# Kernel optimization log

Measured on AMD Instinct MI355X. Metric: run time of the kernel, lower is better.

The kernel has to match this reference:

```python
import jax, jax.numpy as jnp
import numpy as np

N_NODES = 100000
N_EDGES = 1600000
D_IN = 64
D_OUT = 64


def setup_inputs() -> dict:
    key = jax.random.key(0)
    k1, k2, k3, k4 = jax.random.split(key, 4)
    feat = jax.random.normal(k1, (N_NODES, D_IN), dtype=jnp.float32)
    edge_src = jax.random.randint(k2, (N_EDGES,), 0, N_NODES, dtype=jnp.int64)
    edge_dst = jax.random.randint(k3, (N_EDGES,), 0, N_NODES, dtype=jnp.int64)
    # xavier_uniform with gain for relu (sqrt(2)) on [out, in] Linear weight
    gain = float(np.sqrt(2.0))
    limit = gain * float(np.sqrt(6.0 / (D_IN + D_OUT)))
    fc_weight = jax.random.uniform(k4, (D_OUT, D_IN), dtype=jnp.float32,
                                   minval=-limit, maxval=limit)
    return {"feat": feat, "edge_src": edge_src, "edge_dst": edge_dst,
            "fc_weight": fc_weight}


def reference(feat, edge_src, edge_dst, fc_weight):
    # SDDMM: edge score a_e = <h_src, h_dst>  (fn.u_dot_v)
    h_src = feat[edge_src]                      # [E, d]
    h_dst = feat[edge_dst]                      # [E, d]
    a = jnp.sum(h_src * h_dst, axis=-1, keepdims=True)  # [E, 1]
    # SpMM: neigh[v] = sum_{(u->v)} h_u * a_e  (u_mul_e + sum)
    m = h_src * a                               # [E, d]
    neigh = jax.ops.segment_sum(m, edge_dst, num_segments=feat.shape[0])  # [N, d]
    # Linear without bias: y = neigh @ W.T
    return neigh @ fc_weight.T
```

## Files before the change

kernel.cpp:

```cpp
#include <hip/hip_runtime.h>

#define N_NODES 100000
#define N_EDGES 1600000
#define D 64
#define NB 782
#define CAP 4096
#define EPB 8192
#define NPART ((N_EDGES + EPB - 1) / EPB)

__global__ __launch_bounds__(256) void init_gcur(int* __restrict__ gcur) {
    int b = blockIdx.x * 256 + threadIdx.x;
    if (b < NB) gcur[b] = b << 12;
}

__global__ __launch_bounds__(512) void partition(const int* __restrict__ esrc,
                                                 const int* __restrict__ edst,
                                                 int* __restrict__ gcur,
                                                 int* __restrict__ slab) {
    __shared__ int cnt[NB];
    __shared__ int cur[NB];
    const int t = threadIdx.x;
    const int base = blockIdx.x * EPB;
    const int n = min(EPB, N_EDGES - base);

    for (int i = t; i < NB; i += 512) cnt[i] = 0;
    __syncthreads();
    for (int i = t; i < n; i += 512) atomicAdd(&cnt[edst[base + i] >> 7], 1);
    __syncthreads();
    for (int bkt = t; bkt < NB; bkt += 512) {
        const int c = cnt[bkt];
        cur[bkt] = c ? atomicAdd(&gcur[bkt], c) : 0;
    }
    __syncthreads();
    for (int i = t; i < n; i += 512) {
        const int d = edst[base + i];
        const int bkt = d >> 7;
        const int pos = atomicAdd(&cur[bkt], 1);
        if ((pos >> 12) == bkt)
            slab[pos] = ((d & 127) << 17) | esrc[base + i];
    }
}

template<int CTRL>
__device__ __forceinline__ float fadd_dpp(float x) {
    int r = __builtin_amdgcn_update_dpp(0, __float_as_int(x), CTRL, 0xF, 0xF, true);
    return x + __int_as_float(r);
}
__device__ __forceinline__ float row16_allreduce(float p) {
    p = fadd_dpp<0x121>(p);
    p = fadd_dpp<0x122>(p);
    p = fadd_dpp<0x124>(p);
    p = fadd_dpp<0x128>(p);
    return p;
}

__global__ __launch_bounds__(512) void fused_spmm(const float4* __restrict__ feat4,
                                                  const int* __restrict__ slab,
                                                  const int* __restrict__ gcur,
                                                  float4* __restrict__ neigh4) {
    __shared__ int se[CAP];
    __shared__ int cnt[128];
    __shared__ int rowoff[129];
    __shared__ int cur[128];
    const int t = threadIdx.x;
    const int b = blockIdx.x;
    const int nbase = b << 7;
    const int nb_nodes = min(128, N_NODES - nbase);
    const int sbase = b << 12;
    const int ne = min(gcur[b] - sbase, CAP);

    if (t < 128) cnt[t] = 0;
    __syncthreads();
    for (int i = t; i < ne; i += 512)
        atomicAdd(&cnt[slab[sbase + i] >> 17], 1);
    __syncthreads();
    for (int off = 1; off < 128; off <<= 1) {
        const int x = (t >= off && t < 128) ? cnt[t - off] : 0;
        __syncthreads();
        if (t < 128) cnt[t] += x;
        __syncthreads();
    }
    if (t == 0) rowoff[0] = 0;
    if (t < 128) rowoff[t + 1] = cnt[t];
    __syncthreads();
    if (t < 128) cur[t] = rowoff[t];
    __syncthreads();
    for (int i = t; i < ne; i += 512) {
        const int pk = slab[sbase + i];
        const int pos = atomicAdd(&cur[pk >> 17], 1);
        se[pos] = pk & 0x1FFFF;
    }
    __syncthreads();

    const int slot = t >> 4;
    const int l = t & 15;
    for (int ln0 = 0; ln0 < 128; ln0 += 32) {
        const int ln = ln0 + slot;
        if (ln < nb_nodes) {
            const int nidx = nbase + ln;
            const float4 hd = feat4[nidx * 16 + l];
            float ax = 0.f, ay = 0.f, az = 0.f, aw = 0.f;
            int e = rowoff[ln];
            const int e1 = rowoff[ln + 1];
            while (e + 1 < e1) {
                const int s0 = se[e], s1 = se[e + 1];
                const float4 g0 = feat4[s0 * 16 + l];
                const float4 g1 = feat4[s1 * 16 + l];
                float p0 = g0.x * hd.x + g0.y * hd.y + g0.z * hd.z + g0.w * hd.w;
                float p1 = g1.x * hd.x + g1.y * hd.y + g1.z * hd.z + g1.w * hd.w;
                p0 = row16_allreduce(p0);
                p1 = row16_allreduce(p1);
                ax += g0.x * p0 + g1.x * p1;
                ay += g0.y * p0 + g1.y * p1;
                az += g0.z * p0 + g1.z * p1;
                aw += g0.w * p0 + g1.w * p1;
                e += 2;
            }
            if (e < e1) {
                const int s0 = se[e];
                const float4 g0 = feat4[s0 * 16 + l];
                float p0 = g0.x * hd.x + g0.y * hd.y + g0.z * hd.z + g0.w * hd.w;
                p0 = row16_allreduce(p0);
                ax += g0.x * p0;
                ay += g0.y * p0;
                az += g0.z * p0;
                aw += g0.w * p0;
            }
            neigh4[nidx * 16 + l] = make_float4(ax, ay, az, aw);
        }
    }
}

__global__ __launch_bounds__(256) void gemm_inplace(float* __restrict__ out,
                                                    const float* __restrict__ W) {
    __shared__ float WT[64][68];
    __shared__ float nT[64][132];
    const int t = threadIdx.x;

    const float4* W4 = (const float4*)W;
#pragma unroll
    for (int j = 0; j < 4; ++j) {
        const int f = t + j * 256;
        const int o = f >> 4;
        const int i4 = (f & 15) * 4;
        const float4 w = W4[f];
        WT[i4 + 0][o] = w.x;
        WT[i4 + 1][o] = w.y;
        WT[i4 + 2][o] = w.z;
        WT[i4 + 3][o] = w.w;
    }

    const int base = blockIdx.x * 128;
    const int rows = min(128, N_NODES - base);
    const float4* O4 = (const float4*)(out + (long)base * D);
#pragma unroll
    for (int j = 0; j < 8; ++j) {
        const int f = t + j * 256;
        const int r = f >> 4;
        const int i4 = (f & 15) * 4;
        if (r < rows) {
            const float4 x = O4[f];
            nT[i4 + 0][r] = x.x;
            nT[i4 + 1][r] = x.y;
            nT[i4 + 2][r] = x.z;
            nT[i4 + 3][r] = x.w;
        }
    }
    __syncthreads();

    const int c4 = (t & 15) * 4;
    const int r0 = (t >> 4) * 8;
    float acc[8][4];
#pragma unroll
    for (int r = 0; r < 8; ++r)
#pragma unroll
        for (int c = 0; c < 4; ++c) acc[r][c] = 0.f;

    for (int i = 0; i < 64; ++i) {
        const float4 w = *(const float4*)&WT[i][c4];
        const float4 ra = *(const float4*)&nT[i][r0];
        const float4 rb = *(const float4*)&nT[i][r0 + 4];
        const float wv[4] = {w.x, w.y, w.z, w.w};
        const float rv[8] = {ra.x, ra.y, ra.z, ra.w, rb.x, rb.y, rb.z, rb.w};
#pragma unroll
        for (int r = 0; r < 8; ++r)
#pragma unroll
            for (int c = 0; c < 4; ++c) acc[r][c] += rv[r] * wv[c];
    }

#pragma unroll
    for (int r = 0; r < 8; ++r) {
        const int rr = r0 + r;
        if (rr < rows)
            *(float4*)&out[(long)(base + rr) * D + c4] =
                make_float4(acc[r][0], acc[r][1], acc[r][2], acc[r][3]);
    }
}

extern "C" void kernel_launch(void* const* d_in, const int* in_sizes, int n_in,
                              void* d_out, int out_size, void* d_ws, size_t ws_size,
                              hipStream_t stream) {
    const float* feat = (const float*)d_in[0];
    const int*   esrc = (const int*)d_in[1];
    const int*   edst = (const int*)d_in[2];
    const float* W    = (const float*)d_in[3];
    float* out = (float*)d_out;

    char* ws = (char*)d_ws;
    int* slab = (int*)(ws);
    int* gcur = (int*)(ws + (size_t)NB * CAP * 4);

    init_gcur<<<4, 256, 0, stream>>>(gcur);
    partition<<<NPART, 512, 0, stream>>>(esrc, edst, gcur, slab);
    fused_spmm<<<NB, 512, 0, stream>>>((const float4*)feat, slab, gcur, (float4*)out);
    gemm_inplace<<<(N_NODES + 127) / 128, 256, 0, stream>>>(out, W);
}
```

Measured before the change: 191.7 us.

## Gather bf16 source features, sort partition writes by bucket, 8-lane rows

A repack kernel converts feat to bf16 each call, and the SpMM gathers these 128-byte bf16 rows instead of 256-byte fp32 rows, halving gather traffic. Partition now does a block-local prefix scan and stages edges by bucket so slab writes are contiguous. SpMM uses 8 lanes per node with a 3-step DPP reduce and unrolls edges by 4. Bucket capacity is cut from 4096 to 3072. This trades bf16 rounding error in both the score and the message, plus an extra repack pass, for lower memory traffic.

After: 175.0 us. 8.7% less time.

```diff
diff --git a/kernel.cpp b/kernel.cpp
--- a/kernel.cpp
+++ b/kernel.cpp
@@ -4,21 +4,45 @@
 #define N_EDGES 1600000
 #define D 64
 #define NB 782
-#define CAP 4096
+#define CAP 3072
 #define EPB 8192
 #define NPART ((N_EDGES + EPB - 1) / EPB)
 
-__global__ __launch_bounds__(256) void init_gcur(int* __restrict__ gcur) {
-    int b = blockIdx.x * 256 + threadIdx.x;
-    if (b < NB) gcur[b] = b << 12;
+typedef unsigned short ushort_t;
+typedef unsigned int uint_t;
+
+__device__ __forceinline__ ushort_t f2bf(float f) {
+    uint_t u = __float_as_uint(f);
+    u += 0x7FFF + ((u >> 16) & 1);
+    return (ushort_t)(u >> 16);
+}
+
+__global__ __launch_bounds__(256) void repack_init(const float* __restrict__ feat,
+                                                   ushort_t* __restrict__ featb,
+                                                   int* __restrict__ gcur) {
+    const int tid = blockIdx.x * 256 + threadIdx.x;
+    if (tid < NB) gcur[tid] = tid * CAP;
+    const int base = tid * 16;
+    if (base >= N_NODES * D) return;
+    const float4* f4 = (const float4*)(feat + base);
+    ushort4* o4 = (ushort4*)(featb + base);
+#pragma unroll
+    for (int j = 0; j < 4; ++j) {
+        const float4 v = f4[j];
+        o4[j] = make_ushort4(f2bf(v.x), f2bf(v.y), f2bf(v.z), f2bf(v.w));
+    }
 }
 
 __global__ __launch_bounds__(512) void partition(const int* __restrict__ esrc,
                                                  const int* __restrict__ edst,
                                                  int* __restrict__ gcur,
                                                  int* __restrict__ slab) {
+    __shared__ ushort_t stage[EPB];
     __shared__ int cnt[NB];
+    __shared__ int start[NB];
     __shared__ int cur[NB];
+    __shared__ int gb[NB];
+    __shared__ int s[512];
     const int t = threadIdx.x;
     const int base = blockIdx.x * EPB;
     const int n = min(EPB, N_EDGES - base);
@@ -27,34 +51,68 @@
     __syncthreads();
     for (int i = t; i < n; i += 512) atomicAdd(&cnt[edst[base + i] >> 7], 1);
     __syncthreads();
-    for (int bkt = t; bkt < NB; bkt += 512) {
-        const int c = cnt[bkt];
-        cur[bkt] = c ? atomicAdd(&gcur[bkt], c) : 0;
+    int a = 0, b2 = 0;
+    if (2 * t < NB) a = cnt[2 * t];
+    if (2 * t + 1 < NB) b2 = cnt[2 * t + 1];
+    const int sum = a + b2;
+    s[t] = sum;
+    __syncthreads();
+    for (int off = 1; off < 512; off <<= 1) {
+        const int x = (t >= off) ? s[t - off] : 0;
+        __syncthreads();
+        s[t] += x;
+        __syncthreads();
+    }
+    const int excl = s[t] - sum;
+    if (2 * t < NB)     { start[2 * t] = excl;          cur[2 * t] = excl; }
+    if (2 * t + 1 < NB) { start[2 * t + 1] = excl + a;  cur[2 * t + 1] = excl + a; }
+    __syncthreads();
+    for (int k = t; k < NB; k += 512) {
+        const int c = cnt[k];
+        gb[k] = (c ? atomicAdd(&gcur[k], c) : 0) - start[k];
     }
     __syncthreads();
     for (int i = t; i < n; i += 512) {
-        const int d = edst[base + i];
+        const int pos = atomicAdd(&cur[edst[base + i] >> 7], 1);
+        stage[pos] = (ushort_t)i;
+    }
+    __syncthreads();
+    for (int i = t; i < n; i += 512) {
+        const int j = stage[i];
+        const int d = edst[base + j];
         const int bkt = d >> 7;
-        const int pos = atomicAdd(&cur[bkt], 1);
-        if ((pos >> 12) == bkt)
-            slab[pos] = ((d & 127) << 17) | esrc[base + i];
+        const int gp = gb[bkt] + i;
+        if (gp < (bkt + 1) * CAP)
+            slab[gp] = ((d & 127) << 17) | esrc[base + j];
     }
 }
 
 template<int CTRL>
 __device__ __forceinline__ float fadd_dpp(float x) {
-    int r = __builtin_amdgcn_update_dpp(0, __float_as_int(x), CTRL, 0xF, 0xF, true);
+    const int r = __builtin_amdgcn_update_dpp(0, __float_as_int(x), CTRL, 0xF, 0xF, true);
     return x + __int_as_float(r);
 }
-__device__ __forceinline__ float row16_allreduce(float p) {
-    p = fadd_dpp<0x121>(p);
-    p = fadd_dpp<0x122>(p);
-    p = fadd_dpp<0x124>(p);
-    p = fadd_dpp<0x128>(p);
+__device__ __forceinline__ float red8(float p) {
+    p = fadd_dpp<0xB1>(p);
+    p = fadd_dpp<0x4E>(p);
+    p = fadd_dpp<0x141>(p);
     return p;
 }
 
+__device__ __forceinline__ float cvt_dot(const uint4 u, const float* __restrict__ h,
+                                         float* __restrict__ g) {
+    g[0] = __uint_as_float(u.x << 16); g[1] = __uint_as_float(u.x & 0xFFFF0000u);
+    g[2] = __uint_as_float(u.y << 16); g[3] = __uint_as_float(u.y & 0xFFFF0000u);
+    g[4] = __uint_as_float(u.z << 16); g[5] = __uint_as_float(u.z & 0xFFFF0000u);
+    g[6] = __uint_as_float(u.w << 16); g[7] = __uint_as_float(u.w & 0xFFFF0000u);
+    float p = 0.f;
+#pragma unroll
+    for (int k = 0; k < 8; ++k) p += g[k] * h[k];
+    return p;
+}
+
 __global__ __launch_bounds__(512) void fused_spmm(const float4* __restrict__ feat4,
+                                                  const uint4* __restrict__ featb4,
                                                   const int* __restrict__ slab,
                                                   const int* __restrict__ gcur,
                                                   float4* __restrict__ neigh4) {
@@ -66,7 +124,7 @@
     const int b = blockIdx.x;
     const int nbase = b << 7;
     const int nb_nodes = min(128, N_NODES - nbase);
-    const int sbase = b << 12;
+    const int sbase = b * CAP;
     const int ne = min(gcur[b] - sbase, CAP);
 
     if (t < 128) cnt[t] = 0;
@@ -92,42 +150,51 @@
     }
     __syncthreads();
 
-    const int slot = t >> 4;
-    const int l = t & 15;
-    for (int ln0 = 0; ln0 < 128; ln0 += 32) {
+    const int slot = t >> 3;
+    const int l = t & 7;
+#pragma unroll
+    for (int ln0 = 0; ln0 < 128; ln0 += 64) {
         const int ln = ln0 + slot;
-        if (ln < nb_nodes) {
-            const int nidx = nbase + ln;
-            const float4 hd = feat4[nidx * 16 + l];
-            float ax = 0.f, ay = 0.f, az = 0.f, aw = 0.f;
-            int e = rowoff[ln];
-            const int e1 = rowoff[ln + 1];
-            while (e + 1 < e1) {
-                const int s0 = se[e], s1 = se[e + 1];
-                const float4 g0 = feat4[s0 * 16 + l];
-                const float4 g1 = feat4[s1 * 16 + l];
-                float p0 = g0.x * hd.x + g0.y * hd.y + g0.z * hd.z + g0.w * hd.w;
-                float p1 = g1.x * hd.x + g1.y * hd.y + g1.z * hd.z + g1.w * hd.w;
-                p0 = row16_allreduce(p0);
-                p1 = row16_allreduce(p1);
-                ax += g0.x * p0 + g1.x * p1;
-                ay += g0.y * p0 + g1.y * p1;
-                az += g0.z * p0 + g1.z * p1;
-                aw += g0.w * p0 + g1.w * p1;
-                e += 2;
-            }
-            if (e < e1) {
-                const int s0 = se[e];
-                const float4 g0 = feat4[s0 * 16 + l];
-                float p0 = g0.x * hd.x + g0.y * hd.y + g0.z * hd.z + g0.w * hd.w;
-                p0 = row16_allreduce(p0);
-                ax += g0.x * p0;
-                ay += g0.y * p0;
-                az += g0.z * p0;
-                aw += g0.w * p0;
-            }
-            neigh4[nidx * 16 + l] = make_float4(ax, ay, az, aw);
-        }
+        if (ln >= nb_nodes) continue;
+        const int nidx = nbase + ln;
+        float h[8];
+        {
+            const float4 ha = feat4[nidx * 16 + 2 * l];
+            const float4 hb = feat4[nidx * 16 + 2 * l + 1];
+            h[0] = ha.x; h[1] = ha.y; h[2] = ha.z; h[3] = ha.w;
+            h[4] = hb.x; h[5] = hb.y; h[6] = hb.z; h[7] = hb.w;
+        }
+        float acc[8];
+#pragma unroll
+        for (int k = 0; k < 8; ++k) acc[k] = 0.f;
+
+        int e = rowoff[ln];
+        const int e1 = rowoff[ln + 1];
+        for (; e + 3 < e1; e += 4) {
+            const int s0 = se[e], s1 = se[e + 1], s2 = se[e + 2], s3 = se[e + 3];
+            const uint4 u0 = featb4[s0 * 8 + l];
+            const uint4 u1 = featb4[s1 * 8 + l];
+            const uint4 u2 = featb4[s2 * 8 + l];
+            const uint4 u3 = featb4[s3 * 8 + l];
+            float g0[8], g1[8], g2[8], g3[8];
+            float p0 = cvt_dot(u0, h, g0);
+            float p1 = cvt_dot(u1, h, g1);
+            float p2 = cvt_dot(u2, h, g2);
+            float p3 = cvt_dot(u3, h, g3);
+            p0 = red8(p0); p1 = red8(p1); p2 = red8(p2); p3 = red8(p3);
+#pragma unroll
+            for (int k = 0; k < 8; ++k)
+                acc[k] += g0[k] * p0 + g1[k] * p1 + g2[k] * p2 + g3[k] * p3;
+        }
+        for (; e < e1; ++e) {
+            const uint4 u0 = featb4[se[e] * 8 + l];
+            float g0[8];
+            float p0 = red8(cvt_dot(u0, h, g0));
+#pragma unroll
+            for (int k = 0; k < 8; ++k) acc[k] += g0[k] * p0;
+        }
+        neigh4[nidx * 16 + 2 * l]     = make_float4(acc[0], acc[1], acc[2], acc[3]);
+        neigh4[nidx * 16 + 2 * l + 1] = make_float4(acc[4], acc[5], acc[6], acc[7]);
     }
 }
 
@@ -207,11 +274,13 @@
     float* out = (float*)d_out;
 
     char* ws = (char*)d_ws;
-    int* slab = (int*)(ws);
-    int* gcur = (int*)(ws + (size_t)NB * CAP * 4);
-
-    init_gcur<<<4, 256, 0, stream>>>(gcur);
+    ushort_t* featb = (ushort_t*)(ws);
+    int* slab = (int*)(ws + 12800000);
+    int* gcur = (int*)(ws + 12800000 + (size_t)NB * CAP * 4);
+
+    repack_init<<<(N_NODES * D / 16 + 255) / 256, 256, 0, stream>>>(feat, featb, gcur);
     partition<<<NPART, 512, 0, stream>>>(esrc, edst, gcur, slab);
-    fused_spmm<<<NB, 512, 0, stream>>>((const float4*)feat, slab, gcur, (float4*)out);
+    fused_spmm<<<NB, 512, 0, stream>>>((const float4*)feat, (const uint4*)featb,
+                                       slab, gcur, (float4*)out);
     gemm_inplace<<<(N_NODES + 127) / 128, 256, 0, stream>>>(out, W);
 }
```
